# Kernel optimization log

Measured on AMD Instinct MI355X. Metric: run time of the kernel, lower is better.

Reference implementation:

```python
import jax, jax.numpy as jnp
import numpy as np

B, S, H, C = 16, 4096, 1024, 64

def setup_inputs() -> dict:
    key = jax.random.key(0)
    k1, k2 = jax.random.split(key)
    hidden = jax.random.normal(k1, (B, S, H), dtype=jnp.float32)
    querys = jax.random.normal(k2, (C, H), dtype=jnp.float32)
    return {"hidden": hidden, "querys": querys}

def reference(hidden, querys):
    # scores: [B, C, S] = einsum over hidden_size
    scores = jnp.einsum('bsh,ch->bcs', hidden, querys)
    # softmax over the sequence axis
    factor = jax.nn.softmax(scores, axis=2)
    # pooled: [B, C, H]
    result = jnp.einsum('bcs,bsh->bch', factor, hidden)
    # flatten to [B, C*H]
    return result.reshape(-1, querys.shape[0] * querys.shape[1])
```

## Files before the change

### kernel.cpp

```cpp
#include <hip/hip_runtime.h>
#include <math.h>

#define BB 16
#define SS 4096
#define HH 1024
#define CC 64

__global__ __launch_bounds__(256) void scores_kernel(
    const float* __restrict__ hidden, const float* __restrict__ querys,
    float* __restrict__ scores)
{
    const int b  = blockIdx.y;
    const int s0 = blockIdx.x * 64;
    const int t  = threadIdx.x;
    const int tx = t & 15;
    const int ty = t >> 4;
    const int lr  = t >> 4;
    const int lk4 = (t & 15) * 4;

    __shared__ float hs[64][68];
    __shared__ float qs[64][68];

    float acc[4][4];
#pragma unroll
    for (int i = 0; i < 4; ++i)
#pragma unroll
        for (int j = 0; j < 4; ++j) acc[i][j] = 0.0f;

    for (int k0 = 0; k0 < HH; k0 += 64) {
#pragma unroll
        for (int rr = 0; rr < 4; ++rr) {
            const int r = lr + rr * 16;
            const float4 v = *(const float4*)&hidden[((size_t)b * SS + (size_t)(s0 + r)) * HH + k0 + lk4];
            hs[lk4 + 0][r] = v.x; hs[lk4 + 1][r] = v.y;
            hs[lk4 + 2][r] = v.z; hs[lk4 + 3][r] = v.w;
        }
#pragma unroll
        for (int rr = 0; rr < 4; ++rr) {
            const int c = lr + rr * 16;
            const float4 v = *(const float4*)&querys[(size_t)c * HH + k0 + lk4];
            qs[lk4 + 0][c] = v.x; qs[lk4 + 1][c] = v.y;
            qs[lk4 + 2][c] = v.z; qs[lk4 + 3][c] = v.w;
        }
        __syncthreads();
#pragma unroll 8
        for (int k = 0; k < 64; ++k) {
            const float4 a = *(const float4*)&hs[k][ty * 4];
            const float4 q = *(const float4*)&qs[k][tx * 4];
            const float av[4] = {a.x, a.y, a.z, a.w};
            const float qv[4] = {q.x, q.y, q.z, q.w};
#pragma unroll
            for (int i = 0; i < 4; ++i)
#pragma unroll
                for (int j = 0; j < 4; ++j)
                    acc[i][j] = fmaf(av[i], qv[j], acc[i][j]);
        }
        __syncthreads();
    }
#pragma unroll
    for (int j = 0; j < 4; ++j) {
        float4 w;
        w.x = acc[0][j]; w.y = acc[1][j]; w.z = acc[2][j]; w.w = acc[3][j];
        *(float4*)&scores[((size_t)(b * CC + tx * 4 + j)) * SS + s0 + ty * 4] = w;
    }
}

__global__ __launch_bounds__(256) void softmax_kernel(float* __restrict__ scores)
{
    float* p = scores + (size_t)blockIdx.x * SS;
    const int t = threadIdx.x;
    float4 v[4];
    float m = -3.0e38f;
#pragma unroll
    for (int i = 0; i < 4; ++i) {
        v[i] = *(const float4*)&p[t * 4 + i * 1024];
        m = fmaxf(m, fmaxf(fmaxf(v[i].x, v[i].y), fmaxf(v[i].z, v[i].w)));
    }
#pragma unroll
    for (int off = 1; off < 64; off <<= 1) m = fmaxf(m, __shfl_xor(m, off));
    __shared__ float redm[4];
    __shared__ float reds[4];
    const int wave = t >> 6, lane = t & 63;
    if (lane == 0) redm[wave] = m;
    __syncthreads();
    m = fmaxf(fmaxf(redm[0], redm[1]), fmaxf(redm[2], redm[3]));

    float sum = 0.0f;
#pragma unroll
    for (int i = 0; i < 4; ++i) {
        v[i].x = __expf(v[i].x - m); v[i].y = __expf(v[i].y - m);
        v[i].z = __expf(v[i].z - m); v[i].w = __expf(v[i].w - m);
        sum += (v[i].x + v[i].y) + (v[i].z + v[i].w);
    }
#pragma unroll
    for (int off = 1; off < 64; off <<= 1) sum += __shfl_xor(sum, off);
    if (lane == 0) reds[wave] = sum;
    __syncthreads();
    sum = (reds[0] + reds[1]) + (reds[2] + reds[3]);
    const float inv = 1.0f / sum;
#pragma unroll
    for (int i = 0; i < 4; ++i) {
        v[i].x *= inv; v[i].y *= inv; v[i].z *= inv; v[i].w *= inv;
        *(float4*)&p[t * 4 + i * 1024] = v[i];
    }
}

__global__ __launch_bounds__(256) void pool_kernel(
    const float* __restrict__ hidden, const float* __restrict__ factor,
    float* __restrict__ parts)
{
    const int b    = blockIdx.y;
    const int h0   = blockIdx.x * 64;
    const int ks   = blockIdx.z;
    const int sbeg = ks * (SS / 4);
    const int t  = threadIdx.x;
    const int tx = t & 15;
    const int ty = t >> 4;
    const int lr  = t >> 4;
    const int lk4 = (t & 15) * 4;

    __shared__ float fs[64][68];
    __shared__ float hd[64][68];

    float acc[4][4];
#pragma unroll
    for (int i = 0; i < 4; ++i)
#pragma unroll
        for (int j = 0; j < 4; ++j) acc[i][j] = 0.0f;

    for (int sc = 0; sc < SS / 4; sc += 64) {
#pragma unroll
        for (int rr = 0; rr < 4; ++rr) {
            const int c = lr + rr * 16;
            const float4 v = *(const float4*)&factor[((size_t)(b * CC + c)) * SS + sbeg + sc + lk4];
            fs[lk4 + 0][c] = v.x; fs[lk4 + 1][c] = v.y;
            fs[lk4 + 2][c] = v.z; fs[lk4 + 3][c] = v.w;
        }
#pragma unroll
        for (int rr = 0; rr < 4; ++rr) {
            const int r = lr + rr * 16;
            *(float4*)&hd[r][lk4] =
                *(const float4*)&hidden[((size_t)b * SS + (size_t)(sbeg + sc + r)) * HH + h0 + lk4];
        }
        __syncthreads();
#pragma unroll 8
        for (int s = 0; s < 64; ++s) {
            const float4 f = *(const float4*)&fs[s][ty * 4];
            const float4 hv = *(const float4*)&hd[s][tx * 4];
            const float fv[4] = {f.x, f.y, f.z, f.w};
            const float hh[4] = {hv.x, hv.y, hv.z, hv.w};
#pragma unroll
            for (int i = 0; i < 4; ++i)
#pragma unroll
                for (int j = 0; j < 4; ++j)
                    acc[i][j] = fmaf(fv[i], hh[j], acc[i][j]);
        }
        __syncthreads();
    }
    float* dst = parts + (size_t)ks * (BB * CC * HH);
#pragma unroll
    for (int i = 0; i < 4; ++i) {
        float4 w;
        w.x = acc[i][0]; w.y = acc[i][1]; w.z = acc[i][2]; w.w = acc[i][3];
        *(float4*)&dst[(size_t)b * (CC * HH) + (size_t)(ty * 4 + i) * HH + h0 + tx * 4] = w;
    }
}

__global__ __launch_bounds__(256) void reduce4_kernel(
    const float* __restrict__ parts, float* __restrict__ out)
{
    const int i = blockIdx.x * 256 + threadIdx.x;
    const float4* p = (const float4*)parts;
    const float4 a = p[i];
    const float4 b = p[i + 262144];
    const float4 c = p[i + 524288];
    const float4 d = p[i + 786432];
    float4 r;
    r.x = (a.x + b.x) + (c.x + d.x);
    r.y = (a.y + b.y) + (c.y + d.y);
    r.z = (a.z + b.z) + (c.z + d.z);
    r.w = (a.w + b.w) + (c.w + d.w);
    ((float4*)out)[i] = r;
}

extern "C" void kernel_launch(void* const* d_in, const int* in_sizes, int n_in,
                              void* d_out, int out_size, void* d_ws, size_t ws_size,
                              hipStream_t stream)
{
    const float* hidden = (const float*)d_in[0];
    const float* querys = (const float*)d_in[1];
    float* out = (float*)d_out;

    float* scores = (float*)d_ws;
    float* parts  = scores + (size_t)BB * CC * SS;

    scores_kernel<<<dim3(SS / 64, BB), 256, 0, stream>>>(hidden, querys, scores);
    softmax_kernel<<<dim3(BB * CC), 256, 0, stream>>>(scores);
    pool_kernel<<<dim3(HH / 64, BB, 4), 256, 0, stream>>>(hidden, scores, parts);
    reduce4_kernel<<<dim3(1024), 256, 0, stream>>>(parts, out);
}
```

Measured before the change: 540.1 us.

## Move scores and pooling GEMMs onto bf16 MFMA with split-precision scores

Both matmuls now run on MFMA bf16 instructions instead of scalar FP32 FMAs. Scores use a three-term hi/lo bf16 split to keep near-FP32 accuracy, pooling uses single bf16 inputs with the softmax output written as bf16, and global loads are prefetched into registers one tile ahead. The intent is to cut the compute-bound FP32 GEMM time, at the cost of reduced precision in the pooling step and extra conversion work. The workspace is reorganised so scores and parts share the same region.

```diff
diff --git a/kernel.cpp b/kernel.cpp
--- a/kernel.cpp
+++ b/kernel.cpp
@@ -6,68 +6,140 @@
 #define HH 1024
 #define CC 64
 
+typedef __attribute__((ext_vector_type(4))) float f32x4;
+typedef __attribute__((ext_vector_type(8))) short s16x8;
+
+__device__ __forceinline__ ushort f2bf(float x) {
+    union { float f; unsigned u; } un; un.f = x;
+    unsigned r = (un.u + 0x7FFFu + ((un.u >> 16) & 1u)) >> 16;
+    return (ushort)r;
+}
+__device__ __forceinline__ float bf2f(ushort h) {
+    union { unsigned u; float f; } un; un.u = ((unsigned)h) << 16; return un.f;
+}
+
+__global__ __launch_bounds__(256) void prep_querys_kernel(
+    const float* __restrict__ q, ushort* __restrict__ qhi, ushort* __restrict__ qlo)
+{
+    const int i4 = blockIdx.x * 256 + threadIdx.x;
+    const float4 v = ((const float4*)q)[i4];
+    ushort4 h, l;
+    h.x = f2bf(v.x); l.x = f2bf(v.x - bf2f(h.x));
+    h.y = f2bf(v.y); l.y = f2bf(v.y - bf2f(h.y));
+    h.z = f2bf(v.z); l.z = f2bf(v.z - bf2f(h.z));
+    h.w = f2bf(v.w); l.w = f2bf(v.w - bf2f(h.w));
+    ((ushort4*)qhi)[i4] = h;
+    ((ushort4*)qlo)[i4] = l;
+}
+
 __global__ __launch_bounds__(256) void scores_kernel(
-    const float* __restrict__ hidden, const float* __restrict__ querys,
-    float* __restrict__ scores)
-{
+    const float* __restrict__ hidden, const ushort* __restrict__ qhi,
+    const ushort* __restrict__ qlo, float* __restrict__ scores)
+{
+    __shared__ __align__(16) ushort Ahi[128][40];
+    __shared__ __align__(16) ushort Alo[128][40];
+    __shared__ __align__(16) ushort Bhi[64][40];
+    __shared__ __align__(16) ushort Blo[64][40];
+
     const int b  = blockIdx.y;
-    const int s0 = blockIdx.x * 64;
+    const int s0 = blockIdx.x * 128;
     const int t  = threadIdx.x;
-    const int tx = t & 15;
-    const int ty = t >> 4;
-    const int lr  = t >> 4;
-    const int lk4 = (t & 15) * 4;
-
-    __shared__ float hs[64][68];
-    __shared__ float qs[64][68];
-
-    float acc[4][4];
-#pragma unroll
-    for (int i = 0; i < 4; ++i)
-#pragma unroll
-        for (int j = 0; j < 4; ++j) acc[i][j] = 0.0f;
-
-    for (int k0 = 0; k0 < HH; k0 += 64) {
-#pragma unroll
-        for (int rr = 0; rr < 4; ++rr) {
-            const int r = lr + rr * 16;
-            const float4 v = *(const float4*)&hidden[((size_t)b * SS + (size_t)(s0 + r)) * HH + k0 + lk4];
-            hs[lk4 + 0][r] = v.x; hs[lk4 + 1][r] = v.y;
-            hs[lk4 + 2][r] = v.z; hs[lk4 + 3][r] = v.w;
-        }
-#pragma unroll
-        for (int rr = 0; rr < 4; ++rr) {
-            const int c = lr + rr * 16;
-            const float4 v = *(const float4*)&querys[(size_t)c * HH + k0 + lk4];
-            qs[lk4 + 0][c] = v.x; qs[lk4 + 1][c] = v.y;
-            qs[lk4 + 2][c] = v.z; qs[lk4 + 3][c] = v.w;
-        }
-        __syncthreads();
-#pragma unroll 8
-        for (int k = 0; k < 64; ++k) {
-            const float4 a = *(const float4*)&hs[k][ty * 4];
-            const float4 q = *(const float4*)&qs[k][tx * 4];
-            const float av[4] = {a.x, a.y, a.z, a.w};
-            const float qv[4] = {q.x, q.y, q.z, q.w};
-#pragma unroll
-            for (int i = 0; i < 4; ++i)
-#pragma unroll
-                for (int j = 0; j < 4; ++j)
-                    acc[i][j] = fmaf(av[i], qv[j], acc[i][j]);
-        }
-        __syncthreads();
-    }
-#pragma unroll
-    for (int j = 0; j < 4; ++j) {
-        float4 w;
-        w.x = acc[0][j]; w.y = acc[1][j]; w.z = acc[2][j]; w.w = acc[3][j];
-        *(float4*)&scores[((size_t)(b * CC + tx * 4 + j)) * SS + s0 + ty * 4] = w;
-    }
-}
-
-__global__ __launch_bounds__(256) void softmax_kernel(float* __restrict__ scores)
-{
-    float* p = scores + (size_t)blockIdx.x * SS;
+    const int w    = t >> 6;
+    const int lane = t & 63;
+    const int col  = lane & 15;
+    const int quad = lane >> 4;
+    const int lr = t >> 3;
+    const int lc = t & 7;
+
+    f32x4 acc[2][4];
+#pragma unroll
+    for (int i = 0; i < 2; ++i)
+#pragma unroll
+        for (int j = 0; j < 4; ++j) acc[i][j] = (f32x4){0.f, 0.f, 0.f, 0.f};
+
+    const float* hbase = hidden + ((size_t)b * SS + s0) * HH;
+
+    float4 hv[4];
+    ushort4 qh[2], ql[2];
+#pragma unroll
+    for (int p = 0; p < 4; ++p)
+        hv[p] = *(const float4*)&hbase[(size_t)(lr + 32 * p) * HH + lc * 4];
+#pragma unroll
+    for (int p = 0; p < 2; ++p) {
+        qh[p] = ((const ushort4*)qhi)[(lr + 32 * p) * 256 + lc];
+        ql[p] = ((const ushort4*)qlo)[(lr + 32 * p) * 256 + lc];
+    }
+
+    for (int k0 = 0; k0 < HH; k0 += 32) {
+        __syncthreads();
+#pragma unroll
+        for (int p = 0; p < 4; ++p) {
+            const int r = lr + 32 * p;
+            ushort4 h, l;
+            h.x = f2bf(hv[p].x); l.x = f2bf(hv[p].x - bf2f(h.x));
+            h.y = f2bf(hv[p].y); l.y = f2bf(hv[p].y - bf2f(h.y));
+            h.z = f2bf(hv[p].z); l.z = f2bf(hv[p].z - bf2f(h.z));
+            h.w = f2bf(hv[p].w); l.w = f2bf(hv[p].w - bf2f(h.w));
+            *(ushort4*)&Ahi[r][lc * 4] = h;
+            *(ushort4*)&Alo[r][lc * 4] = l;
+        }
+#pragma unroll
+        for (int p = 0; p < 2; ++p) {
+            *(ushort4*)&Bhi[lr + 32 * p][lc * 4] = qh[p];
+            *(ushort4*)&Blo[lr + 32 * p][lc * 4] = ql[p];
+        }
+        __syncthreads();
+
+        if (k0 + 32 < HH) {
+            const int kn = k0 + 32;
+#pragma unroll
+            for (int p = 0; p < 4; ++p)
+                hv[p] = *(const float4*)&hbase[(size_t)(lr + 32 * p) * HH + kn + lc * 4];
+#pragma unroll
+            for (int p = 0; p < 2; ++p) {
+                qh[p] = ((const ushort4*)qhi)[(lr + 32 * p) * 256 + kn / 4 + lc];
+                ql[p] = ((const ushort4*)qlo)[(lr + 32 * p) * 256 + kn / 4 + lc];
+            }
+        }
+
+        s16x8 ah[2], al[2], bh[4], bl[4];
+#pragma unroll
+        for (int mt = 0; mt < 2; ++mt) {
+            const int r = w * 32 + mt * 16 + col;
+            ah[mt] = *(const s16x8*)&Ahi[r][quad * 8];
+            al[mt] = *(const s16x8*)&Alo[r][quad * 8];
+        }
+#pragma unroll
+        for (int nt = 0; nt < 4; ++nt) {
+            const int r = nt * 16 + col;
+            bh[nt] = *(const s16x8*)&Bhi[r][quad * 8];
+            bl[nt] = *(const s16x8*)&Blo[r][quad * 8];
+        }
+#pragma unroll
+        for (int mt = 0; mt < 2; ++mt)
+#pragma unroll
+            for (int nt = 0; nt < 4; ++nt) {
+                acc[mt][nt] = __builtin_amdgcn_mfma_f32_16x16x32_bf16(ah[mt], bh[nt], acc[mt][nt], 0, 0, 0);
+                acc[mt][nt] = __builtin_amdgcn_mfma_f32_16x16x32_bf16(ah[mt], bl[nt], acc[mt][nt], 0, 0, 0);
+                acc[mt][nt] = __builtin_amdgcn_mfma_f32_16x16x32_bf16(al[mt], bh[nt], acc[mt][nt], 0, 0, 0);
+            }
+    }
+
+#pragma unroll
+    for (int mt = 0; mt < 2; ++mt)
+#pragma unroll
+        for (int nt = 0; nt < 4; ++nt) {
+            const int c = nt * 16 + col;
+            const int s = s0 + w * 32 + mt * 16 + quad * 4;
+            *(f32x4*)&scores[((size_t)(b * CC + c)) * SS + s] = acc[mt][nt];
+        }
+}
+
+__global__ __launch_bounds__(256) void softmax_kernel(
+    const float* __restrict__ scores, ushort* __restrict__ factor)
+{
+    const float* p = scores + (size_t)blockIdx.x * SS;
+    ushort* f = factor + (size_t)blockIdx.x * SS;
     const int t = threadIdx.x;
     float4 v[4];
     float m = -3.0e38f;
@@ -100,69 +172,91 @@
     const float inv = 1.0f / sum;
 #pragma unroll
     for (int i = 0; i < 4; ++i) {
-        v[i].x *= inv; v[i].y *= inv; v[i].z *= inv; v[i].w *= inv;
-        *(float4*)&p[t * 4 + i * 1024] = v[i];
+        ushort4 o;
+        o.x = f2bf(v[i].x * inv); o.y = f2bf(v[i].y * inv);
+        o.z = f2bf(v[i].z * inv); o.w = f2bf(v[i].w * inv);
+        ((ushort4*)f)[t + i * 256] = o;
     }
 }
 
 __global__ __launch_bounds__(256) void pool_kernel(
-    const float* __restrict__ hidden, const float* __restrict__ factor,
+    const float* __restrict__ hidden, const ushort* __restrict__ factor,
     float* __restrict__ parts)
 {
-    const int b    = blockIdx.y;
-    const int h0   = blockIdx.x * 64;
-    const int ks   = blockIdx.z;
+    __shared__ __align__(16) ushort Ht[64][72];
+
+    const int b  = blockIdx.y;
+    const int h0 = blockIdx.x * 64;
+    const int ks = blockIdx.z;
     const int sbeg = ks * (SS / 4);
-    const int t  = threadIdx.x;
-    const int tx = t & 15;
-    const int ty = t >> 4;
-    const int lr  = t >> 4;
-    const int lk4 = (t & 15) * 4;
-
-    __shared__ float fs[64][68];
-    __shared__ float hd[64][68];
-
-    float acc[4][4];
-#pragma unroll
-    for (int i = 0; i < 4; ++i)
-#pragma unroll
-        for (int j = 0; j < 4; ++j) acc[i][j] = 0.0f;
+    const int t = threadIdx.x;
+    const int w = t >> 6, lane = t & 63, col = lane & 15, quad = lane >> 4;
+    const int hc = t & 15;
+    const int sq = t >> 4;
+
+    f32x4 acc[4];
+#pragma unroll
+    for (int j = 0; j < 4; ++j) acc[j] = (f32x4){0.f, 0.f, 0.f, 0.f};
+
+    const float* hbase = hidden + (size_t)b * SS * HH + h0;
+    const ushort* fbase = factor + (size_t)(b * CC + w * 16 + col) * SS + sbeg;
+
+    float v[16];
+#pragma unroll
+    for (int pp = 0; pp < 2; ++pp)
+#pragma unroll
+        for (int mm = 0; mm < 4; ++mm)
+#pragma unroll
+            for (int e = 0; e < 2; ++e)
+                v[pp * 8 + mm * 2 + e] =
+                    hbase[(size_t)(sbeg + 2 * (sq + 16 * pp) + e) * HH + hc + 16 * mm];
 
     for (int sc = 0; sc < SS / 4; sc += 64) {
-#pragma unroll
-        for (int rr = 0; rr < 4; ++rr) {
-            const int c = lr + rr * 16;
-            const float4 v = *(const float4*)&factor[((size_t)(b * CC + c)) * SS + sbeg + sc + lk4];
-            fs[lk4 + 0][c] = v.x; fs[lk4 + 1][c] = v.y;
-            fs[lk4 + 2][c] = v.z; fs[lk4 + 3][c] = v.w;
-        }
-#pragma unroll
-        for (int rr = 0; rr < 4; ++rr) {
-            const int r = lr + rr * 16;
-            *(float4*)&hd[r][lk4] =
-                *(const float4*)&hidden[((size_t)b * SS + (size_t)(sbeg + sc + r)) * HH + h0 + lk4];
-        }
-        __syncthreads();
-#pragma unroll 8
-        for (int s = 0; s < 64; ++s) {
-            const float4 f = *(const float4*)&fs[s][ty * 4];
-            const float4 hv = *(const float4*)&hd[s][tx * 4];
-            const float fv[4] = {f.x, f.y, f.z, f.w};
-            const float hh[4] = {hv.x, hv.y, hv.z, hv.w};
-#pragma unroll
-            for (int i = 0; i < 4; ++i)
-#pragma unroll
-                for (int j = 0; j < 4; ++j)
-                    acc[i][j] = fmaf(fv[i], hh[j], acc[i][j]);
-        }
-        __syncthreads();
-    }
-    float* dst = parts + (size_t)ks * (BB * CC * HH);
-#pragma unroll
-    for (int i = 0; i < 4; ++i) {
-        float4 w;
-        w.x = acc[i][0]; w.y = acc[i][1]; w.z = acc[i][2]; w.w = acc[i][3];
-        *(float4*)&dst[(size_t)b * (CC * HH) + (size_t)(ty * 4 + i) * HH + h0 + tx * 4] = w;
+        __syncthreads();
+#pragma unroll
+        for (int pp = 0; pp < 2; ++pp)
+#pragma unroll
+            for (int mm = 0; mm < 4; ++mm) {
+                unsigned pack = (unsigned)f2bf(v[pp * 8 + mm * 2 + 0]) |
+                                ((unsigned)f2bf(v[pp * 8 + mm * 2 + 1]) << 16);
+                ((unsigned*)Ht)[(hc + 16 * mm) * 36 + (sq + 16 * pp)] = pack;
+            }
+        __syncthreads();
+
+        const s16x8 fa0 = *(const s16x8*)&fbase[sc + quad * 8];
+        const s16x8 fa1 = *(const s16x8*)&fbase[sc + 32 + quad * 8];
+
+        if (sc + 64 < SS / 4) {
+#pragma unroll
+            for (int pp = 0; pp < 2; ++pp)
+#pragma unroll
+                for (int mm = 0; mm < 4; ++mm)
+#pragma unroll
+                    for (int e = 0; e < 2; ++e)
+                        v[pp * 8 + mm * 2 + e] =
+                            hbase[(size_t)(sbeg + sc + 64 + 2 * (sq + 16 * pp) + e) * HH + hc + 16 * mm];
+        }
+
+#pragma unroll
+        for (int ksp = 0; ksp < 2; ++ksp) {
+            const s16x8 fa = ksp ? fa1 : fa0;
+#pragma unroll
+            for (int nt = 0; nt < 4; ++nt) {
+                const s16x8 hb = *(const s16x8*)&Ht[nt * 16 + col][ksp * 32 + quad * 8];
+                acc[nt] = __builtin_amdgcn_mfma_f32_16x16x32_bf16(fa, hb, acc[nt], 0, 0, 0);
+            }
+        }
+    }
+
+    float* dst = parts + (size_t)ks * (BB * CC * HH) + (size_t)b * (CC * HH);
+#pragma unroll
+    for (int nt = 0; nt < 4; ++nt) {
+        const int h = h0 + nt * 16 + col;
+#pragma unroll
+        for (int r = 0; r < 4; ++r) {
+            const int c = w * 16 + quad * 4 + r;
+            dst[(size_t)c * HH + h] = acc[nt][r];
+        }
     }
 }
 
@@ -191,11 +285,15 @@
     const float* querys = (const float*)d_in[1];
     float* out = (float*)d_out;
 
-    float* scores = (float*)d_ws;
-    float* parts  = scores + (size_t)BB * CC * SS;
-
-    scores_kernel<<<dim3(SS / 64, BB), 256, 0, stream>>>(hidden, querys, scores);
-    softmax_kernel<<<dim3(BB * CC), 256, 0, stream>>>(scores);
-    pool_kernel<<<dim3(HH / 64, BB, 4), 256, 0, stream>>>(hidden, scores, parts);
+    float*  scores = (float*)d_ws;
+    float*  parts  = (float*)d_ws;
+    ushort* factor = (ushort*)((char*)d_ws + (16u << 20));
+    ushort* qhi    = (ushort*)((char*)d_ws + (24u << 20));
+    ushort* qlo    = qhi + CC * HH;
+
+    prep_querys_kernel<<<dim3(CC * HH / 1024), 256, 0, stream>>>(querys, qhi, qlo);
+    scores_kernel<<<dim3(SS / 128, BB), 256, 0, stream>>>(hidden, qhi, qlo, scores);
+    softmax_kernel<<<dim3(BB * CC), 256, 0, stream>>>(scores, factor);
+    pool_kernel<<<dim3(HH / 64, BB, 4), 256, 0, stream>>>(hidden, factor, parts);
     reduce4_kernel<<<dim3(1024), 256, 0, stream>>>(parts, out);
 }
```

Result: faster. 455.6 us (-15.6%).
